# Optimization experiments

Hardware: AMD Instinct MI355X
Metric: run time of the kernel (lower is better)

The kernel has to match this reference:

```python
import jax, jax.numpy as jnp
import numpy as np

NUM_LAYERS = 4
NUM_HEADS = 8
D_MODEL = 256
D_FF = 1024
UNC_THRESHOLD = 0.3
B, L = 2, 2048


def _layer_norm(x, g, b, eps=1e-5):
    m = jnp.mean(x, axis=-1, keepdims=True)
    v = jnp.mean((x - m) ** 2, axis=-1, keepdims=True)
    return (x - m) * jax.lax.rsqrt(v + eps) * g + b


def setup_inputs() -> dict:
    key = jax.random.key(0)
    ks = jax.random.split(key, 32)
    D, F, Ly = D_MODEL, D_FF, NUM_LAYERS
    w = lambda k, shape: jax.random.normal(k, shape, dtype=jnp.float32) * 0.02
    return {
        'x': jax.random.normal(ks[0], (B, L, D), dtype=jnp.float32),
        'Win': w(ks[1], (D, D)), 'bin_': jnp.zeros((D,), jnp.float32),
        'Wq': w(ks[2], (Ly, D, D)), 'bq': jnp.zeros((Ly, D), jnp.float32),
        'Wk': w(ks[3], (Ly, D, D)), 'bk': jnp.zeros((Ly, D), jnp.float32),
        'Wv': w(ks[4], (Ly, D, D)), 'bv': jnp.zeros((Ly, D), jnp.float32),
        'Wo': w(ks[5], (Ly, D, D)), 'bo': jnp.zeros((Ly, D), jnp.float32),
        'ev_scale': jnp.ones((Ly,), jnp.float32),
        'ev_bias': jnp.zeros((Ly,), jnp.float32),
        'W1': w(ks[6], (Ly, D, F)), 'b1': jnp.zeros((Ly, F), jnp.float32),
        'W2': w(ks[7], (Ly, F, D)), 'b2': jnp.zeros((Ly, D), jnp.float32),
        'n1g': jnp.ones((Ly, D), jnp.float32), 'n1b': jnp.zeros((Ly, D), jnp.float32),
        'n2g': jnp.ones((Ly, D), jnp.float32), 'n2b': jnp.zeros((Ly, D), jnp.float32),
        'fng': jnp.ones((D,), jnp.float32), 'fnb': jnp.zeros((D,), jnp.float32),
        'Wout': w(ks[8], (D, D)), 'bout': jnp.zeros((D,), jnp.float32),
    }


def _evidence_attention(x, Wq, bq, Wk, bk, Wv, bv, Wo, bo, scale, bias):
    b, l, d = x.shape
    hd = d // NUM_HEADS
    def heads(t):
        return t.reshape(b, l, NUM_HEADS, hd).transpose(0, 2, 1, 3)  # [B,H,L,hd]
    Q = heads(x @ Wq + bq)
    K = heads(x @ Wk + bk)
    V = heads(x @ Wv + bv)
    scores = jnp.einsum('bhqd,bhkd->bhqk', Q, K) / np.sqrt(hd).astype(np.float32)
    evidence = jnp.exp(scores) * scale + 1.0 + bias           # [B,H,L,L]
    denom = jnp.sum(evidence, axis=-1, keepdims=True)         # [B,H,L,1]
    uncertainty = (jnp.float32(l) / denom)[..., 0]            # [B,H,L]
    probs = evidence / denom
    attn = jnp.einsum('bhqk,bhkd->bhqd', probs, V)
    attn = attn.transpose(0, 2, 1, 3).reshape(b, l, d)
    return attn @ Wo + bo, uncertainty


def reference(x, Win, bin_, Wq, bq, Wk, bk, Wv, bv, Wo, bo, ev_scale, ev_bias,
              W1, b1, W2, b2, n1g, n1b, n2g, n2b, fng, fnb, Wout, bout):
    h = x @ Win + bin_
    total_unc = 0.0
    for i in range(NUM_LAYERS):
        attn_out, unc = _evidence_attention(
            _layer_norm(h, n1g[i], n1b[i]),
            Wq[i], bq[i], Wk[i], bk[i], Wv[i], bv[i], Wo[i], bo[i],
            ev_scale[i], ev_bias[i])
        h = h + attn_out
        ff = jax.nn.gelu(_layer_norm(h, n2g[i], n2b[i]) @ W1[i] + b1[i], approximate=False) @ W2[i] + b2[i]
        h = h + ff
        total_unc = total_unc + unc
    avg_unc = total_unc / NUM_LAYERS                          # [B,H,L]
    out = _layer_norm(h, fng, fnb) @ Wout + bout              # [B,L,D]
    should_abstain = avg_unc > UNC_THRESHOLD
    return out, avg_unc, should_abstain
```

## Files before the change

### kernel.cpp

```cpp
#include <hip/hip_runtime.h>
#include <hip/hip_bf16.h>
#include <math.h>

#define B_  2
#define L_  2048
#define D_  256
#define H_  8
#define HD_ 32
#define F_  1024
#define LY_ 4
#define M_  (B_*L_)

typedef __attribute__((ext_vector_type(8))) short bf16x8;
typedef __attribute__((ext_vector_type(4))) float f32x4;

static __device__ __forceinline__ short f2bf(float f) {
    return __builtin_bit_cast(short, __float2bfloat16(f));
}

__global__ __launch_bounds__(256) void transpose_weights(
    const float* __restrict__ Win, const float* __restrict__ Wq,
    const float* __restrict__ Wk,  const float* __restrict__ Wv,
    const float* __restrict__ Wo,  const float* __restrict__ W1,
    const float* __restrict__ W2,  const float* __restrict__ Wout,
    ushort* __restrict__ T)
{
    const int bid = blockIdx.x;
    const float* src; ushort* dst; int K, N, tt;
    if (bid < 64)        { src = Win; dst = T; K = 256; N = 256; tt = bid; }
    else if (bid < 1088) {
        int i = bid - 64; int which = i >> 8; int l = (i >> 6) & 3; tt = i & 63;
        K = 256; N = 256;
        const float* s4[4] = {Wq, Wk, Wv, Wo};
        src = s4[which] + l * 65536;
        dst = T + 65536 * (1 + which * 4 + l);
    } else if (bid < 2112) {
        int i = bid - 1088; int l = i >> 8; tt = i & 255; K = 256; N = 1024;
        src = W1 + l * 262144; dst = T + 65536 * 17 + l * 262144;
    } else if (bid < 3136) {
        int i = bid - 2112; int l = i >> 8; tt = i & 255; K = 1024; N = 256;
        src = W2 + l * 262144; dst = T + 65536 * 17 + 1048576 + l * 262144;
    } else {
        src = Wout; dst = T + 65536 * 17 + 2097152; K = 256; N = 256; tt = bid - 3136;
    }
    const int ntn = N >> 5;
    const int tk = tt / ntn, tn = tt % ntn;
    __shared__ float ld[32][33];
    const int t = threadIdx.x;
    const int r = t >> 3, c4 = (t & 7) * 4;
    float4 v = *reinterpret_cast<const float4*>(&src[(size_t)(tk * 32 + r) * N + tn * 32 + c4]);
    ld[r][c4 + 0] = v.x; ld[r][c4 + 1] = v.y; ld[r][c4 + 2] = v.z; ld[r][c4 + 3] = v.w;
    __syncthreads();
    short4 o;
    o.x = f2bf(ld[c4 + 0][r]);
    o.y = f2bf(ld[c4 + 1][r]);
    o.z = f2bf(ld[c4 + 2][r]);
    o.w = f2bf(ld[c4 + 3][r]);
    *reinterpret_cast<short4*>(&dst[(size_t)(tn * 32 + r) * K + tk * 32 + c4]) = o;
}

__global__ __launch_bounds__(256) void f32_to_bf16(
    const float* __restrict__ in, ushort* __restrict__ out)
{
    const int i = (blockIdx.x * 256 + threadIdx.x) * 4;
    float4 v = *reinterpret_cast<const float4*>(&in[i]);
    short4 o = {f2bf(v.x), f2bf(v.y), f2bf(v.z), f2bf(v.w)};
    *reinterpret_cast<short4*>(&out[i]) = o;
}

__device__ __forceinline__ void gemm_core64(
    const ushort* __restrict__ A, const ushort* __restrict__ Wt, int K,
    int row0, int col0, ushort* sA, ushort* sW, f32x4 acc[2][2])
{
    const int tid  = threadIdx.x;
    const int lane = tid & 63;
    const int wid  = tid >> 6;
    const int wr = wid >> 1, wc = wid & 1;
    const int g = lane >> 4, nn = lane & 15;
    const int srow = tid >> 2;
    const int sch  = (tid & 3) * 16;

    const ushort* Ap = &A[(size_t)(row0 + srow) * K + sch];
    const ushort* Wp = &Wt[(size_t)(col0 + srow) * K + sch];

    for (int k0 = 0; k0 < K; k0 += 64) {
        bf16x8 av0 = *reinterpret_cast<const bf16x8*>(Ap + k0);
        bf16x8 av1 = *reinterpret_cast<const bf16x8*>(Ap + k0 + 8);
        bf16x8 wv0 = *reinterpret_cast<const bf16x8*>(Wp + k0);
        bf16x8 wv1 = *reinterpret_cast<const bf16x8*>(Wp + k0 + 8);
        __syncthreads();
        *reinterpret_cast<bf16x8*>(&sA[srow * 72 + sch])     = av0;
        *reinterpret_cast<bf16x8*>(&sA[srow * 72 + sch + 8]) = av1;
        *reinterpret_cast<bf16x8*>(&sW[srow * 72 + sch])     = wv0;
        *reinterpret_cast<bf16x8*>(&sW[srow * 72 + sch + 8]) = wv1;
        __syncthreads();
#pragma unroll
        for (int s = 0; s < 2; ++s) {
            bf16x8 a0 = *reinterpret_cast<const bf16x8*>(&sA[(wr * 32 + nn) * 72 + s * 32 + g * 8]);
            bf16x8 a1 = *reinterpret_cast<const bf16x8*>(&sA[(wr * 32 + 16 + nn) * 72 + s * 32 + g * 8]);
            bf16x8 w0 = *reinterpret_cast<const bf16x8*>(&sW[(wc * 32 + nn) * 72 + s * 32 + g * 8]);
            bf16x8 w1 = *reinterpret_cast<const bf16x8*>(&sW[(wc * 32 + 16 + nn) * 72 + s * 32 + g * 8]);
            acc[0][0] = __builtin_amdgcn_mfma_f32_16x16x32_bf16(a0, w0, acc[0][0], 0, 0, 0);
            acc[0][1] = __builtin_amdgcn_mfma_f32_16x16x32_bf16(a0, w1, acc[0][1], 0, 0, 0);
            acc[1][0] = __builtin_amdgcn_mfma_f32_16x16x32_bf16(a1, w0, acc[1][0], 0, 0, 0);
            acc[1][1] = __builtin_amdgcn_mfma_f32_16x16x32_bf16(a1, w1, acc[1][1], 0, 0, 0);
        }
    }
}

template<int EPI, int OUTBF>
__global__ __launch_bounds__(256) void gemm_bf16(
    const ushort* __restrict__ A, const ushort* __restrict__ Wt,
    const float* __restrict__ bias, const float* __restrict__ res,
    void* __restrict__ Cout, int M, int N, int K)
{
    __shared__ __align__(16) ushort sA[64 * 72];
    __shared__ __align__(16) ushort sW[64 * 72];
    const int row0 = blockIdx.y * 64, col0 = blockIdx.x * 64;
    f32x4 acc[2][2] = {};
    gemm_core64(A, Wt, K, row0, col0, sA, sW, acc);

    const int lane = threadIdx.x & 63;
    const int wid  = threadIdx.x >> 6;
    const int wr = wid >> 1, wc = wid & 1;
    const int g = lane >> 4, nn = lane & 15;
#pragma unroll
    for (int mi = 0; mi < 2; ++mi)
#pragma unroll
    for (int ni = 0; ni < 2; ++ni)
#pragma unroll
    for (int r = 0; r < 4; ++r) {
        const int m = row0 + wr * 32 + mi * 16 + g * 4 + r;
        const int c = col0 + wc * 32 + ni * 16 + nn;
        float v = acc[mi][ni][r] + bias[c];
        if (EPI == 1) v = 0.5f * v * (1.0f + erff(v * 0.70710678118654752f));
        if (EPI == 2) v += res[(size_t)m * N + c];
        if (OUTBF) ((ushort*)Cout)[(size_t)m * N + c] = (ushort)f2bf(v);
        else       ((float*)Cout)[(size_t)m * N + c] = v;
    }
}

__global__ __launch_bounds__(256) void gemm_qkv(
    const ushort* __restrict__ A,
    const ushort* __restrict__ WqT, const ushort* __restrict__ WkT,
    const ushort* __restrict__ WvT,
    const float* __restrict__ bq, const float* __restrict__ bk,
    const float* __restrict__ bv,
    ushort* __restrict__ Qb, ushort* __restrict__ Kb, ushort* __restrict__ Vt)
{
    __shared__ __align__(16) ushort sA[64 * 72];
    __shared__ __align__(16) ushort sW[64 * 72];
    const int nb = blockIdx.x;
    const int wsel = nb >> 2;
    const int col0 = (nb & 3) * 64;
    const int row0 = blockIdx.y * 64;
    const ushort* Wt = (wsel == 0) ? WqT : (wsel == 1) ? WkT : WvT;
    const float* bias = (wsel == 0) ? bq : (wsel == 1) ? bk : bv;

    f32x4 acc[2][2] = {};
    gemm_core64(A, Wt, 256, row0, col0, sA, sW, acc);

    const int lane = threadIdx.x & 63;
    const int wid  = threadIdx.x >> 6;
    const int wr = wid >> 1, wc = wid & 1;
    const int g = lane >> 4, nn = lane & 15;
    ushort* QK = (wsel == 0) ? Qb : Kb;
#pragma unroll
    for (int mi = 0; mi < 2; ++mi)
#pragma unroll
    for (int ni = 0; ni < 2; ++ni)
#pragma unroll
    for (int r = 0; r < 4; ++r) {
        const int m = row0 + wr * 32 + mi * 16 + g * 4 + r;
        const int c = col0 + wc * 32 + ni * 16 + nn;
        const float v = acc[mi][ni][r] + bias[c];
        if (wsel < 2) {
            QK[(size_t)m * D_ + c] = (ushort)f2bf(v);
        } else {
            const int b = m >> 11, l = m & 2047;
            const int h = c >> 5,  d = c & 31;
            Vt[(size_t)((b * 8 + h) * 32 + d) * L_ + l] = (ushort)f2bf(v);
        }
    }
}

__global__ __launch_bounds__(256) void ln_kernel(
    const float* __restrict__ x, const float* __restrict__ g,
    const float* __restrict__ b, ushort* __restrict__ y)
{
    const int row = blockIdx.x;
    const int tid = threadIdx.x;
    const float v = x[row * D_ + tid];
    float s = v, s2 = v * v;
#pragma unroll
    for (int off = 32; off > 0; off >>= 1) {
        s  += __shfl_xor(s,  off);
        s2 += __shfl_xor(s2, off);
    }
    __shared__ float ls[4], ls2[4];
    const int wid = tid >> 6;
    if ((tid & 63) == 0) { ls[wid] = s; ls2[wid] = s2; }
    __syncthreads();
    s  = ls[0]  + ls[1]  + ls[2]  + ls[3];
    s2 = ls2[0] + ls2[1] + ls2[2] + ls2[3];
    const float m   = s * (1.0f / D_);
    const float var = s2 * (1.0f / D_) - m * m;
    const float r   = rsqrtf(var + 1e-5f);
    y[row * D_ + tid] = (ushort)f2bf((v - m) * r * g[tid] + b[tid]);
}

__global__ __launch_bounds__(256) void attn_mfma(
    const ushort* __restrict__ Qb, const ushort* __restrict__ Kb,
    const ushort* __restrict__ Vt, ushort* __restrict__ O,
    float* __restrict__ unc, const float* __restrict__ ev_scale,
    const float* __restrict__ ev_bias, int layer)
{
    const int bh = blockIdx.y;
    const int b  = bh >> 3;
    const int h  = bh & 7;
    const int tid  = threadIdx.x;
    const int wv   = tid >> 6;
    const int lane = tid & 63;
    const int g = lane >> 4;
    const int n = lane & 15;
    const int q  = blockIdx.x * 64 + wv * 16 + n;
    const float scale = ev_scale[layer];
    const float cb    = 1.0f + ev_bias[layer];
    const float isq   = 0.17677669529663687f;

    __shared__ __align__(16) ushort sK[2][64][40];
    __shared__ __align__(16) ushort sV[2][32][72];

    const size_t qk0 = (size_t)b * L_ * D_ + h * HD_;
    const bf16x8 qf = *reinterpret_cast<const bf16x8*>(&Qb[qk0 + (size_t)q * D_ + g * 8]);

    const int krow = tid >> 2, kch = (tid & 3) * 8;
    const int vrow = tid >> 3, vch = (tid & 7) * 8;
    const ushort* ksrc = Kb + qk0 + (size_t)krow * D_ + kch;
    const ushort* vsrc = Vt + (size_t)((b * 8 + h) * 32 + vrow) * L_ + vch;

    f32x4 acc0 = {0.f, 0.f, 0.f, 0.f};
    f32x4 acc1 = {0.f, 0.f, 0.f, 0.f};
    const f32x4 zero = {0.f, 0.f, 0.f, 0.f};
    float esum = 0.f;

    bf16x8 kreg = *reinterpret_cast<const bf16x8*>(ksrc);
    bf16x8 vreg = *reinterpret_cast<const bf16x8*>(vsrc);

    int cur = 0;
    for (int t = 0; t < L_; t += 64) {
        *reinterpret_cast<bf16x8*>(&sK[cur][krow][kch]) = kreg;
        *reinterpret_cast<bf16x8*>(&sV[cur][vrow][vch]) = vreg;
        if (t + 64 < L_) {
            kreg = *reinterpret_cast<const bf16x8*>(ksrc + (size_t)(t + 64) * D_);
            vreg = *reinterpret_cast<const bf16x8*>(vsrc + (t + 64));
        }
        __syncthreads();

#pragma unroll
        for (int tt = 0; tt < 64; tt += 32) {
            bf16x8 kf0 = *reinterpret_cast<const bf16x8*>(&sK[cur][tt + n][g * 8]);
            bf16x8 kf1 = *reinterpret_cast<const bf16x8*>(&sK[cur][tt + 16 + n][g * 8]);

            f32x4 s0 = __builtin_amdgcn_mfma_f32_16x16x32_bf16(kf0, qf, zero, 0, 0, 0);
            f32x4 s1 = __builtin_amdgcn_mfma_f32_16x16x32_bf16(kf1, qf, zero, 0, 0, 0);

            short4 va = *reinterpret_cast<const short4*>(&sV[cur][n][tt + g * 4]);
            short4 vb = *reinterpret_cast<const short4*>(&sV[cur][n][tt + 16 + g * 4]);
            short4 vc = *reinterpret_cast<const short4*>(&sV[cur][n + 16][tt + g * 4]);
            short4 vd = *reinterpret_cast<const short4*>(&sV[cur][n + 16][tt + 16 + g * 4]);
            bf16x8 vf0 = {va.x, va.y, va.z, va.w, vb.x, vb.y, vb.z, vb.w};
            bf16x8 vf1 = {vc.x, vc.y, vc.z, vc.w, vd.x, vd.y, vd.z, vd.w};

            bf16x8 pa;
#pragma unroll
            for (int r = 0; r < 4; ++r) {
                float e = fmaf(__expf(s0[r] * isq), scale, cb);
                esum += e;
                pa[r] = f2bf(e);
            }
#pragma unroll
            for (int r = 0; r < 4; ++r) {
                float e = fmaf(__expf(s1[r] * isq), scale, cb);
                esum += e;
                pa[r + 4] = f2bf(e);
            }

            acc0 = __builtin_amdgcn_mfma_f32_16x16x32_bf16(vf0, pa, acc0, 0, 0, 0);
            acc1 = __builtin_amdgcn_mfma_f32_16x16x32_bf16(vf1, pa, acc1, 0, 0, 0);
        }
        cur ^= 1;
    }

    esum += __shfl_xor(esum, 16);
    esum += __shfl_xor(esum, 32);
    const float inv = 1.0f / esum;

    ushort* op = &O[qk0 + (size_t)q * D_ + g * 4];
    short4 o0 = {f2bf(acc0[0] * inv), f2bf(acc0[1] * inv), f2bf(acc0[2] * inv), f2bf(acc0[3] * inv)};
    short4 o1 = {f2bf(acc1[0] * inv), f2bf(acc1[1] * inv), f2bf(acc1[2] * inv), f2bf(acc1[3] * inv)};
    *reinterpret_cast<short4*>(op)      = o0;
    *reinterpret_cast<short4*>(op + 16) = o1;

    if (g == 0) {
        const float u = (float)L_ * inv;
        const int uidx = bh * L_ + q;
        unc[uidx] = (layer == 0) ? u : (unc[uidx] + u);
    }
}

__global__ __launch_bounds__(256) void unc_final(
    const float* __restrict__ unc, float* __restrict__ out_unc,
    float* __restrict__ out_abst)
{
    const int i = blockIdx.x * 256 + threadIdx.x;
    const float u = unc[i] * 0.25f;
    out_unc[i]  = u;
    out_abst[i] = (u > 0.3f) ? 1.0f : 0.0f;
}

extern "C" void kernel_launch(void* const* d_in, const int* in_sizes, int n_in,
                              void* d_out, int out_size, void* d_ws, size_t ws_size,
                              hipStream_t stream)
{
    const float* x    = (const float*)d_in[0];
    const float* Win  = (const float*)d_in[1];
    const float* bin_ = (const float*)d_in[2];
    const float* Wq   = (const float*)d_in[3];
    const float* bq   = (const float*)d_in[4];
    const float* Wk   = (const float*)d_in[5];
    const float* bk   = (const float*)d_in[6];
    const float* Wv   = (const float*)d_in[7];
    const float* bv   = (const float*)d_in[8];
    const float* Wo   = (const float*)d_in[9];
    const float* bo   = (const float*)d_in[10];
    const float* evs  = (const float*)d_in[11];
    const float* evb  = (const float*)d_in[12];
    const float* W1   = (const float*)d_in[13];
    const float* b1   = (const float*)d_in[14];
    const float* W2   = (const float*)d_in[15];
    const float* b2   = (const float*)d_in[16];
    const float* n1g  = (const float*)d_in[17];
    const float* n1b  = (const float*)d_in[18];
    const float* n2g  = (const float*)d_in[19];
    const float* n2b  = (const float*)d_in[20];
    const float* fng  = (const float*)d_in[21];
    const float* fnb  = (const float*)d_in[22];
    const float* Wout = (const float*)d_in[23];
    const float* bout = (const float*)d_in[24];

    char* ws = (char*)d_ws;
    float*  h    = (float*) (ws);
    ushort* tmpb = (ushort*)(ws + (4  << 20));
    ushort* Qb   = (ushort*)(ws + (6  << 20));
    ushort* Kb   = (ushort*)(ws + (8  << 20));
    ushort* Vt   = (ushort*)(ws + (10 << 20));
    ushort* Ob   = (ushort*)(ws + (12 << 20));
    ushort* ffb  = (ushort*)(ws + (6  << 20));
    float*  unc  = (float*) (ws + (14 << 20));
    ushort* T    = (ushort*)(ws + (15 << 20));

    ushort* winT  = T;
    ushort* woutT = T + 65536 * 17 + 2097152;

    float* out_main = (float*)d_out;
    float* out_unc  = out_main + M_ * D_;
    float* out_abst = out_unc + B_ * H_ * L_;

    const dim3 blk(256);
    const dim3 g256(4, 64);
    const dim3 g1024(16, 64);
    const dim3 gqkv(12, 64);
    const dim3 gattn(L_ / 64, B_ * H_);

    transpose_weights<<<3200, blk, 0, stream>>>(Win, Wq, Wk, Wv, Wo, W1, W2, Wout, T);
    f32_to_bf16<<<1024, blk, 0, stream>>>(x, tmpb);
    gemm_bf16<0, 0><<<g256, blk, 0, stream>>>(tmpb, winT, bin_, nullptr, h, M_, D_, D_);

    for (int i = 0; i < LY_; ++i) {
        ushort* wqT = T + 65536 * (1 + i);
        ushort* wkT = T + 65536 * (5 + i);
        ushort* wvT = T + 65536 * (9 + i);
        ushort* woT = T + 65536 * (13 + i);
        ushort* w1T = T + 65536 * 17 + i * 262144;
        ushort* w2T = T + 65536 * 17 + 1048576 + i * 262144;

        ln_kernel<<<M_, blk, 0, stream>>>(h, n1g + i * D_, n1b + i * D_, tmpb);
        gemm_qkv<<<gqkv, blk, 0, stream>>>(tmpb, wqT, wkT, wvT,
                                           bq + i * D_, bk + i * D_, bv + i * D_,
                                           Qb, Kb, Vt);
        attn_mfma<<<gattn, blk, 0, stream>>>(Qb, Kb, Vt, Ob, unc, evs, evb, i);
        gemm_bf16<2, 0><<<g256, blk, 0, stream>>>(Ob, woT, bo + i * D_, h, h, M_, D_, D_);
        ln_kernel<<<M_, blk, 0, stream>>>(h, n2g + i * D_, n2b + i * D_, tmpb);
        gemm_bf16<1, 1><<<g1024, blk, 0, stream>>>(tmpb, w1T, b1 + i * F_, nullptr, ffb, M_, F_, D_);
        gemm_bf16<2, 0><<<g256, blk, 0, stream>>>(ffb, w2T, b2 + i * D_, h, h, M_, D_, F_);
    }

    ln_kernel<<<M_, blk, 0, stream>>>(h, fng, fnb, tmpb);
    gemm_bf16<0, 0><<<g256, blk, 0, stream>>>(tmpb, woutT, bout, nullptr, out_main, M_, D_, D_);
    unc_final<<<(B_ * H_ * L_) / 256, blk, 0, stream>>>(unc, out_unc, out_abst);
}
```

Before: 312.1 us.

## Use direct global-to-LDS loads with double buffering and MFMA row sums

The GEMM core now loads tiles straight into LDS with global_load_lds, double-buffers them, and uses an XOR swizzle in place of padding. This removes the register round trip and halves the number of barriers per K step. The attention kernel folds the 1/sqrt(hd) scale into Q and computes the evidence row sum with an extra MFMA against a ones vector instead of scalar adds and shuffles. The denominator now sums bf16-rounded evidence, which slightly changes numerics, and the doubled LDS footprint per block may lower occupancy.

```diff
diff --git a/kernel.cpp b/kernel.cpp
--- a/kernel.cpp
+++ b/kernel.cpp
@@ -16,6 +16,12 @@
 
 static __device__ __forceinline__ short f2bf(float f) {
     return __builtin_bit_cast(short, __float2bfloat16(f));
+}
+
+static __device__ __forceinline__ void gload_lds16(const ushort* g, ushort* l) {
+    __builtin_amdgcn_global_load_lds(
+        (const __attribute__((address_space(1))) void*)g,
+        (__attribute__((address_space(3))) void*)l, 16, 0, 0);
 }
 
 __global__ __launch_bounds__(256) void transpose_weights(
@@ -77,34 +83,53 @@
     const int wid  = tid >> 6;
     const int wr = wid >> 1, wc = wid & 1;
     const int g = lane >> 4, nn = lane & 15;
-    const int srow = tid >> 2;
-    const int sch  = (tid & 3) * 16;
-
-    const ushort* Ap = &A[(size_t)(row0 + srow) * K + sch];
-    const ushort* Wp = &Wt[(size_t)(col0 + srow) * K + sch];
-
+
+    const int r0 = tid >> 3;
+    const int sx = ((tid & 7) ^ (r0 & 7)) << 3;
+
+    const ushort* Ap = &A[(size_t)(row0 + r0) * K + sx];
+    const ushort* Wp = &Wt[(size_t)(col0 + r0) * K + sx];
+    const size_t rstep = (size_t)32 * K;
+
+    ushort* ldsA = sA + wid * 512;
+    ushort* ldsW = sW + wid * 512;
+
+    gload_lds16(Ap,         ldsA);
+    gload_lds16(Ap + rstep, ldsA + 2048);
+    gload_lds16(Wp,         ldsW);
+    gload_lds16(Wp + rstep, ldsW + 2048);
+
+    const int ra = (wr * 32 + nn) * 64, rb = ra + 16 * 64;
+    const int rc = (wc * 32 + nn) * 64, rd = rc + 16 * 64;
+    const int m7 = nn & 7;
+
+    int cur = 0;
+    __syncthreads();
     for (int k0 = 0; k0 < K; k0 += 64) {
-        bf16x8 av0 = *reinterpret_cast<const bf16x8*>(Ap + k0);
-        bf16x8 av1 = *reinterpret_cast<const bf16x8*>(Ap + k0 + 8);
-        bf16x8 wv0 = *reinterpret_cast<const bf16x8*>(Wp + k0);
-        bf16x8 wv1 = *reinterpret_cast<const bf16x8*>(Wp + k0 + 8);
-        __syncthreads();
-        *reinterpret_cast<bf16x8*>(&sA[srow * 72 + sch])     = av0;
-        *reinterpret_cast<bf16x8*>(&sA[srow * 72 + sch + 8]) = av1;
-        *reinterpret_cast<bf16x8*>(&sW[srow * 72 + sch])     = wv0;
-        *reinterpret_cast<bf16x8*>(&sW[srow * 72 + sch + 8]) = wv1;
-        __syncthreads();
-#pragma unroll
-        for (int s = 0; s < 2; ++s) {
-            bf16x8 a0 = *reinterpret_cast<const bf16x8*>(&sA[(wr * 32 + nn) * 72 + s * 32 + g * 8]);
-            bf16x8 a1 = *reinterpret_cast<const bf16x8*>(&sA[(wr * 32 + 16 + nn) * 72 + s * 32 + g * 8]);
-            bf16x8 w0 = *reinterpret_cast<const bf16x8*>(&sW[(wc * 32 + nn) * 72 + s * 32 + g * 8]);
-            bf16x8 w1 = *reinterpret_cast<const bf16x8*>(&sW[(wc * 32 + 16 + nn) * 72 + s * 32 + g * 8]);
+        if (k0 + 64 < K) {
+            ushort* lA = ldsA + (cur ^ 1) * 4096;
+            ushort* lW = ldsW + (cur ^ 1) * 4096;
+            gload_lds16(Ap + k0 + 64,         lA);
+            gload_lds16(Ap + k0 + 64 + rstep, lA + 2048);
+            gload_lds16(Wp + k0 + 64,         lW);
+            gload_lds16(Wp + k0 + 64 + rstep, lW + 2048);
+        }
+        const ushort* a = sA + cur * 4096;
+        const ushort* w = sW + cur * 4096;
+#pragma unroll
+        for (int sk = 0; sk < 2; ++sk) {
+            const int sw = ((sk * 4 + g) ^ m7) << 3;
+            bf16x8 a0 = *reinterpret_cast<const bf16x8*>(&a[ra + sw]);
+            bf16x8 a1 = *reinterpret_cast<const bf16x8*>(&a[rb + sw]);
+            bf16x8 w0 = *reinterpret_cast<const bf16x8*>(&w[rc + sw]);
+            bf16x8 w1 = *reinterpret_cast<const bf16x8*>(&w[rd + sw]);
             acc[0][0] = __builtin_amdgcn_mfma_f32_16x16x32_bf16(a0, w0, acc[0][0], 0, 0, 0);
             acc[0][1] = __builtin_amdgcn_mfma_f32_16x16x32_bf16(a0, w1, acc[0][1], 0, 0, 0);
             acc[1][0] = __builtin_amdgcn_mfma_f32_16x16x32_bf16(a1, w0, acc[1][0], 0, 0, 0);
             acc[1][1] = __builtin_amdgcn_mfma_f32_16x16x32_bf16(a1, w1, acc[1][1], 0, 0, 0);
         }
+        __syncthreads();
+        cur ^= 1;
     }
 }
 
@@ -114,8 +139,8 @@
     const float* __restrict__ bias, const float* __restrict__ res,
     void* __restrict__ Cout, int M, int N, int K)
 {
-    __shared__ __align__(16) ushort sA[64 * 72];
-    __shared__ __align__(16) ushort sW[64 * 72];
+    __shared__ __align__(16) ushort sA[2 * 4096];
+    __shared__ __align__(16) ushort sW[2 * 4096];
     const int row0 = blockIdx.y * 64, col0 = blockIdx.x * 64;
     f32x4 acc[2][2] = {};
     gemm_core64(A, Wt, K, row0, col0, sA, sW, acc);
@@ -148,8 +173,8 @@
     const float* __restrict__ bv,
     ushort* __restrict__ Qb, ushort* __restrict__ Kb, ushort* __restrict__ Vt)
 {
-    __shared__ __align__(16) ushort sA[64 * 72];
-    __shared__ __align__(16) ushort sW[64 * 72];
+    __shared__ __align__(16) ushort sA[2 * 4096];
+    __shared__ __align__(16) ushort sW[2 * 4096];
     const int nb = blockIdx.x;
     const int wsel = nb >> 2;
     const int col0 = (nb & 3) * 64;
@@ -232,7 +257,19 @@
     __shared__ __align__(16) ushort sV[2][32][72];
 
     const size_t qk0 = (size_t)b * L_ * D_ + h * HD_;
-    const bf16x8 qf = *reinterpret_cast<const bf16x8*>(&Qb[qk0 + (size_t)q * D_ + g * 8]);
+
+    bf16x8 qf;
+    {
+        const bf16x8 qr = *reinterpret_cast<const bf16x8*>(&Qb[qk0 + (size_t)q * D_ + g * 8]);
+#pragma unroll
+        for (int j = 0; j < 8; ++j) {
+            const float qv = __builtin_bit_cast(float, ((unsigned)(unsigned short)qr[j]) << 16);
+            qf[j] = f2bf(qv * isq);
+        }
+    }
+    bf16x8 ones;
+#pragma unroll
+    for (int j = 0; j < 8; ++j) ones[j] = (short)0x3F80;
 
     const int krow = tid >> 2, kch = (tid & 3) * 8;
     const int vrow = tid >> 3, vch = (tid & 7) * 8;
@@ -241,8 +278,8 @@
 
     f32x4 acc0 = {0.f, 0.f, 0.f, 0.f};
     f32x4 acc1 = {0.f, 0.f, 0.f, 0.f};
+    f32x4 accS = {0.f, 0.f, 0.f, 0.f};
     const f32x4 zero = {0.f, 0.f, 0.f, 0.f};
-    float esum = 0.f;
 
     bf16x8 kreg = *reinterpret_cast<const bf16x8*>(ksrc);
     bf16x8 vreg = *reinterpret_cast<const bf16x8*>(vsrc);
@@ -274,27 +311,18 @@
 
             bf16x8 pa;
 #pragma unroll
-            for (int r = 0; r < 4; ++r) {
-                float e = fmaf(__expf(s0[r] * isq), scale, cb);
-                esum += e;
-                pa[r] = f2bf(e);
-            }
-#pragma unroll
-            for (int r = 0; r < 4; ++r) {
-                float e = fmaf(__expf(s1[r] * isq), scale, cb);
-                esum += e;
-                pa[r + 4] = f2bf(e);
-            }
+            for (int r = 0; r < 4; ++r) pa[r]     = f2bf(fmaf(__expf(s0[r]), scale, cb));
+#pragma unroll
+            for (int r = 0; r < 4; ++r) pa[r + 4] = f2bf(fmaf(__expf(s1[r]), scale, cb));
 
             acc0 = __builtin_amdgcn_mfma_f32_16x16x32_bf16(vf0, pa, acc0, 0, 0, 0);
             acc1 = __builtin_amdgcn_mfma_f32_16x16x32_bf16(vf1, pa, acc1, 0, 0, 0);
+            accS = __builtin_amdgcn_mfma_f32_16x16x32_bf16(ones, pa, accS, 0, 0, 0);
         }
         cur ^= 1;
     }
 
-    esum += __shfl_xor(esum, 16);
-    esum += __shfl_xor(esum, 32);
-    const float inv = 1.0f / esum;
+    const float inv = 1.0f / accS[0];
 
     ushort* op = &O[qk0 + (size_t)q * D_ + g * 4];
     short4 o0 = {f2bf(acc0[0] * inv), f2bf(acc0[1] * inv), f2bf(acc0[2] * inv), f2bf(acc0[3] * inv)};
```

Result: faster. 301.5 us (-3.4%).
